# Performance work log

Measured on AMD Instinct MI355X. Metric: run time of the kernel, lower is better.

## Reference

```python
import jax, jax.numpy as jnp
import numpy as np

N_PAPER = 100000
N_AUTHOR = 50000
D = 128
UNITS = 128
E = 500000


def setup_inputs() -> dict:
    key = jax.random.key(0)
    ks = jax.random.split(key, 10)
    s = 1.0 / np.sqrt(D)
    return {
        "x_paper": jax.random.normal(ks[0], (N_PAPER, D), jnp.float32),
        "x_author": jax.random.normal(ks[1], (N_AUTHOR, D), jnp.float32),
        "W_cites": jax.random.normal(ks[2], (D, UNITS), jnp.float32) * s,
        "W_writes": jax.random.normal(ks[3], (D, UNITS), jnp.float32) * s,
        "W_self": jax.random.normal(ks[4], (D, UNITS), jnp.float32) * s,
        "bias": jnp.zeros((UNITS,), jnp.float32),
        "cites_src": jax.random.randint(ks[5], (E,), 0, N_PAPER, jnp.int32),
        "cites_dst": jax.random.randint(ks[6], (E,), 0, N_PAPER, jnp.int32),
        "writes_src": jax.random.randint(ks[7], (E,), 0, N_AUTHOR, jnp.int32),
        "writes_dst": jax.random.randint(ks[8], (E,), 0, N_PAPER, jnp.int32),
    }


def reference(x_paper, x_author, W_cites, W_writes, W_self, bias,
              cites_src, cites_dst, writes_src, writes_dst) -> jnp.ndarray:
    n_recv = x_paper.shape[0]

    # Per-edge-set: transform sender node states, gather to edges, segment-sum to receivers.
    def pool(x_sender, W, src, dst):
        h = x_sender @ W                                  # [n_sender, units]
        msgs = jnp.take(h, src, axis=0)                   # [E, units] broadcast to edges
        pooled = jax.ops.segment_sum(msgs, dst, num_segments=n_recv)
        deg = jax.ops.segment_sum(jnp.ones_like(dst, jnp.float32), dst,
                                  num_segments=n_recv)
        return pooled, deg

    pooled_c, deg_c = pool(x_paper, W_cites, cites_src, cites_dst)
    pooled_w, deg_w = pool(x_author, W_writes, writes_src, writes_dst)

    # Self-loop transform counts as one more "in-edge" per node for mean.
    self_vals = x_paper @ W_self                          # [n_recv, units]
    summed = pooled_c + pooled_w + self_vals
    total_deg = deg_c + deg_w + 1.0                       # [n_recv]

    # tf.math.divide_no_nan semantics
    mean = jnp.where(total_deg[:, None] != 0.0, summed / total_deg[:, None], 0.0)
    return jax.nn.relu(mean + bias)
```

## Files before the change

kernel.cpp:

```cpp
#include <hip/hip_runtime.h>
#include <hip/hip_bf16.h>

#define NP     100000
#define NA     50000
#define DIM    128
#define UNITS  128
#define NEDGE  500000
#define NE2    (2 * NEDGE)

#define BM   128
#define GPB  ((NP + BM - 1) / BM)
#define GAB  ((NA + BM - 1) / BM)

#define CHUNK  1024
#define NCHUNK ((NP + CHUNK - 1) / CHUNK)

typedef __attribute__((ext_vector_type(8))) short bfrag;
typedef __attribute__((ext_vector_type(4))) float f32x4;

__device__ __forceinline__ unsigned int bf_rne(float x) {
    unsigned int u = __builtin_bit_cast(unsigned int, x);
    u += 0x7FFFu + ((u >> 16) & 1u);
    return u >> 16;
}
__device__ __forceinline__ float bf_to_f(unsigned int b) {
    unsigned int u = b << 16;
    return __builtin_bit_cast(float, u);
}

__global__ __launch_bounds__(256, 1) void mfma_gemm_all(
    const float* __restrict__ x_paper, const float* __restrict__ x_author,
    const float* __restrict__ W_cites, const float* __restrict__ W_writes,
    const float* __restrict__ W_self,
    float* __restrict__ H, float* __restrict__ out)
{
    const float* X; const float* W; float* Ho; int nrows; int bb;
    if (blockIdx.x < GPB) {
        X = x_paper;  W = W_cites;  Ho = H;                      nrows = NP; bb = blockIdx.x;
    } else if (blockIdx.x < GPB + GAB) {
        X = x_author; W = W_writes; Ho = H + (size_t)NP * UNITS; nrows = NA; bb = blockIdx.x - GPB;
    } else {
        X = x_paper;  W = W_self;   Ho = out;                    nrows = NP; bb = blockIdx.x - GPB - GAB;
    }

    __shared__ unsigned short Xhi[BM * DIM];
    __shared__ unsigned short Xlo[BM * DIM];
    __shared__ unsigned short Whi[DIM * UNITS];
    __shared__ unsigned short Wlo[DIM * UNITS];

    const int tid  = threadIdx.x;
    const int row0 = bb * BM;

#pragma unroll
    for (int i = 0; i < 8; ++i) {
        const int item = i * 256 + tid;
        const int n    = item & 127;
        const int koct = item >> 7;
        unsigned int h[8], l[8];
#pragma unroll
        for (int j = 0; j < 8; ++j) {
            const float e = W[(size_t)(koct * 8 + j) * UNITS + n];
            h[j] = bf_rne(e);
            l[j] = bf_rne(e - bf_to_f(h[j]));
        }
        uint4 hv, lv;
        hv.x = h[0] | (h[1] << 16); hv.y = h[2] | (h[3] << 16);
        hv.z = h[4] | (h[5] << 16); hv.w = h[6] | (h[7] << 16);
        lv.x = l[0] | (l[1] << 16); lv.y = l[2] | (l[3] << 16);
        lv.z = l[4] | (l[5] << 16); lv.w = l[6] | (l[7] << 16);
        const int slot = koct * 128 + n;
        ((uint4*)Whi)[slot] = hv;
        ((uint4*)Wlo)[slot] = lv;
    }

    const float4* X4 = (const float4*)(X + (size_t)row0 * DIM);
#pragma unroll
    for (int i = 0; i < 8; ++i) {
        const int item = i * 256 + tid;
        const int koct = item & 15;
        const int row  = item >> 4;
        if (row0 + row < nrows) {
            const float4 v0 = X4[row * 32 + koct * 2];
            const float4 v1 = X4[row * 32 + koct * 2 + 1];
            const float e[8] = {v0.x, v0.y, v0.z, v0.w, v1.x, v1.y, v1.z, v1.w};
            unsigned int h[8], l[8];
#pragma unroll
            for (int j = 0; j < 8; ++j) {
                h[j] = bf_rne(e[j]);
                l[j] = bf_rne(e[j] - bf_to_f(h[j]));
            }
            uint4 hv, lv;
            hv.x = h[0] | (h[1] << 16); hv.y = h[2] | (h[3] << 16);
            hv.z = h[4] | (h[5] << 16); hv.w = h[6] | (h[7] << 16);
            lv.x = l[0] | (l[1] << 16); lv.y = l[2] | (l[3] << 16);
            lv.z = l[4] | (l[5] << 16); lv.w = l[6] | (l[7] << 16);
            const int slot = koct * 128 + (row ^ koct);
            ((uint4*)Xhi)[slot] = hv;
            ((uint4*)Xlo)[slot] = lv;
        }
    }
    __syncthreads();

    const int lane = tid & 63;
    const int wv   = tid >> 6;
    const int wr   = (wv >> 1) * 64;
    const int wc   = (wv & 1) * 64;
    const int l16  = lane & 15;
    const int q    = lane >> 4;

    f32x4 acc[4][4];
#pragma unroll
    for (int rt = 0; rt < 4; ++rt)
#pragma unroll
        for (int ct = 0; ct < 4; ++ct) acc[rt][ct] = (f32x4)(0.0f);

#pragma unroll
    for (int kk = 0; kk < 4; ++kk) {
        const int fb = kk * 4 + q;
        bfrag ah[4], al[4], bh[4], bl[4];
#pragma unroll
        for (int rt = 0; rt < 4; ++rt) {
            const int row = wr + rt * 16 + l16;
            const int off = (fb * 128 + (row ^ fb)) * 8;
            ah[rt] = *(const bfrag*)&Xhi[off];
            al[rt] = *(const bfrag*)&Xlo[off];
        }
#pragma unroll
        for (int ct = 0; ct < 4; ++ct) {
            const int off = (fb * 128 + wc + ct * 16 + l16) * 8;
            bh[ct] = *(const bfrag*)&Whi[off];
            bl[ct] = *(const bfrag*)&Wlo[off];
        }
#pragma unroll
        for (int rt = 0; rt < 4; ++rt)
#pragma unroll
            for (int ct = 0; ct < 4; ++ct) {
                acc[rt][ct] = __builtin_amdgcn_mfma_f32_16x16x32_bf16(
                    ah[rt], bh[ct], acc[rt][ct], 0, 0, 0);
                acc[rt][ct] = __builtin_amdgcn_mfma_f32_16x16x32_bf16(
                    ah[rt], bl[ct], acc[rt][ct], 0, 0, 0);
                acc[rt][ct] = __builtin_amdgcn_mfma_f32_16x16x32_bf16(
                    al[rt], bh[ct], acc[rt][ct], 0, 0, 0);
            }
    }

#pragma unroll
    for (int rt = 0; rt < 4; ++rt) {
#pragma unroll
        for (int r = 0; r < 4; ++r) {
            const int row = wr + rt * 16 + q * 4 + r;
            if (row0 + row < nrows) {
                float* dst = Ho + (size_t)(row0 + row) * UNITS + wc + l16;
#pragma unroll
                for (int ct = 0; ct < 4; ++ct) dst[ct * 16] = acc[rt][ct][r];
            }
        }
    }
}

__global__ __launch_bounds__(256) void zero_count(int* __restrict__ count)
{
    int i = blockIdx.x * 256 + threadIdx.x;
    if (i < NP) count[i] = 0;
}

__global__ __launch_bounds__(256) void hist_k(
    const int* __restrict__ c_dst, const int* __restrict__ w_dst,
    int* __restrict__ count)
{
    int i = blockIdx.x * 256 + threadIdx.x;
    if (i >= NE2) return;
    int d = (i < NEDGE) ? c_dst[i] : w_dst[i - NEDGE];
    atomicAdd(&count[d], 1);
}

__global__ __launch_bounds__(256) void scanA(
    const int* __restrict__ count, int* __restrict__ csum)
{
    __shared__ int red[256];
    const int c = blockIdx.x, t = threadIdx.x;
    const int base = c * CHUNK + t * 4;
    int s = 0;
#pragma unroll
    for (int r = 0; r < 4; ++r)
        if (base + r < NP) s += count[base + r];
    red[t] = s; __syncthreads();
#pragma unroll
    for (int off = 128; off > 0; off >>= 1) {
        if (t < off) red[t] += red[t + off];
        __syncthreads();
    }
    if (t == 0) csum[c] = red[0];
}

__global__ __launch_bounds__(128) void scanB(
    const int* __restrict__ csum, int* __restrict__ coff)
{
    __shared__ int ts[128];
    const int t = threadIdx.x;
    const int v = (t < NCHUNK) ? csum[t] : 0;
    ts[t] = v; __syncthreads();
    for (int off = 1; off < 128; off <<= 1) {
        int x = (t >= off) ? ts[t - off] : 0;
        __syncthreads();
        ts[t] += x;
        __syncthreads();
    }
    if (t < NCHUNK) coff[t] = ts[t] - v;
}

__global__ __launch_bounds__(256) void scanC(
    const int* __restrict__ count, const int* __restrict__ coff,
    int* __restrict__ cursor)
{
    __shared__ int ts[256];
    const int c = blockIdx.x, t = threadIdx.x;
    const int base = c * CHUNK + t * 4;
    int v0 = 0, v1 = 0, v2 = 0, v3 = 0;
    if (base + 0 < NP) v0 = count[base + 0];
    if (base + 1 < NP) v1 = count[base + 1];
    if (base + 2 < NP) v2 = count[base + 2];
    if (base + 3 < NP) v3 = count[base + 3];
    const int s = v0 + v1 + v2 + v3;
    ts[t] = s; __syncthreads();
    for (int off = 1; off < 256; off <<= 1) {
        int x = (t >= off) ? ts[t - off] : 0;
        __syncthreads();
        ts[t] += x;
        __syncthreads();
    }
    int excl = ts[t] - s + coff[c];
    if (base + 0 < NP) cursor[base + 0] = excl;
    if (base + 1 < NP) cursor[base + 1] = excl + v0;
    if (base + 2 < NP) cursor[base + 2] = excl + v0 + v1;
    if (base + 3 < NP) cursor[base + 3] = excl + v0 + v1 + v2;
}

__global__ __launch_bounds__(256) void fill_k(
    const int* __restrict__ c_src, const int* __restrict__ c_dst,
    const int* __restrict__ w_src, const int* __restrict__ w_dst,
    int* __restrict__ cursor, int* __restrict__ eidx)
{
    int i = blockIdx.x * 256 + threadIdx.x;
    if (i >= NE2) return;
    int d, val;
    if (i < NEDGE) { d = c_dst[i];         val = c_src[i]; }
    else           { int j = i - NEDGE; d = w_dst[j]; val = NP + w_src[j]; }
    int pos = atomicAdd(&cursor[d], 1);
    eidx[pos] = val;
}

__global__ __launch_bounds__(256) void gather_fused(
    const float* __restrict__ H, const int* __restrict__ eidx,
    const int* __restrict__ cursor, const float* __restrict__ bias,
    float* __restrict__ out)
{
    const int tid = threadIdx.x;
    const int g = tid >> 5, l = tid & 31;
    const int n = blockIdx.x * 8 + g;

    float4 acc = ((const float4*)out)[(size_t)n * 32 + l];

    const int start = (n == 0) ? 0 : cursor[n - 1];
    const int end   = cursor[n];
    const float4* H4 = (const float4*)H;
    int e_next = (start < end) ? eidx[start] : 0;
    for (int j = start; j < end; ++j) {
        const int e = e_next;
        if (j + 1 < end) e_next = eidx[j + 1];
        const float4 v = H4[(size_t)e * 32 + l];
        acc.x += v.x; acc.y += v.y; acc.z += v.z; acc.w += v.w;
    }

    const float inv = 1.0f / (float)(end - start + 1);
    const float4 b = ((const float4*)bias)[l];
    float4 o;
    o.x = fmaxf(fmaf(acc.x, inv, b.x), 0.0f);
    o.y = fmaxf(fmaf(acc.y, inv, b.y), 0.0f);
    o.z = fmaxf(fmaf(acc.z, inv, b.z), 0.0f);
    o.w = fmaxf(fmaf(acc.w, inv, b.w), 0.0f);
    ((float4*)out)[(size_t)n * 32 + l] = o;
}

extern "C" void kernel_launch(void* const* d_in, const int* in_sizes, int n_in,
                              void* d_out, int out_size, void* d_ws, size_t ws_size,
                              hipStream_t stream)
{
    const float* x_paper    = (const float*)d_in[0];
    const float* x_author   = (const float*)d_in[1];
    const float* W_cites    = (const float*)d_in[2];
    const float* W_writes   = (const float*)d_in[3];
    const float* W_self     = (const float*)d_in[4];
    const float* bias       = (const float*)d_in[5];
    const int*   cites_src  = (const int*)d_in[6];
    const int*   cites_dst  = (const int*)d_in[7];
    const int*   writes_src = (const int*)d_in[8];
    const int*   writes_dst = (const int*)d_in[9];
    float* out = (float*)d_out;

    char* ws = (char*)d_ws;
    float* H      = (float*)(ws);
    int*   eidx   = (int*)(ws + 76800000);
    int*   count  = (int*)(ws + 80800000);
    int*   cursor = (int*)(ws + 81200000);
    int*   csum   = (int*)(ws + 81600000);
    int*   coff   = (int*)(ws + 81600512);

    mfma_gemm_all<<<2 * GPB + GAB, 256, 0, stream>>>(
        x_paper, x_author, W_cites, W_writes, W_self, H, out);

    zero_count<<<(NP + 255) / 256, 256, 0, stream>>>(count);
    hist_k<<<(NE2 + 255) / 256, 256, 0, stream>>>(cites_dst, writes_dst, count);
    scanA<<<NCHUNK, 256, 0, stream>>>(count, csum);
    scanB<<<1, 128, 0, stream>>>(csum, coff);
    scanC<<<NCHUNK, 256, 0, stream>>>(count, coff, cursor);
    fill_k<<<(NE2 + 255) / 256, 256, 0, stream>>>(
        cites_src, cites_dst, writes_src, writes_dst, cursor, eidx);

    gather_fused<<<NP / 8, 256, 0, stream>>>(H, eidx, cursor, bias, out);
}
```

Measured before the change: 393.9 us.

## Prepack weights once, load via global_load_lds, merge scan kernels, unroll gather

A new small kernel converts each weight matrix into split-bf16 hi/lo form once and also zeroes the histogram counts. The GEMM blocks then copy the packed weights straight into LDS with global_load_lds instead of each block redoing the float-to-bf16 split. The middle scan pass is folded into the final scan kernel, where every block recomputes the chunk-offset prefix, removing a launch. The gather loop is unrolled by two with two accumulators to keep more loads in flight. The cost is an extra workspace buffer and redundant per-block prefix work.

```diff
diff --git a/kernel.cpp b/kernel.cpp
--- a/kernel.cpp
+++ b/kernel.cpp
@@ -18,6 +18,9 @@
 typedef __attribute__((ext_vector_type(8))) short bfrag;
 typedef __attribute__((ext_vector_type(4))) float f32x4;
 
+typedef const __attribute__((address_space(1))) unsigned int* gptr_u32;
+typedef __attribute__((address_space(3))) unsigned int*       lptr_u32;
+
 __device__ __forceinline__ unsigned int bf_rne(float x) {
     unsigned int u = __builtin_bit_cast(unsigned int, x);
     u += 0x7FFFu + ((u >> 16) & 1u);
@@ -27,50 +30,77 @@
     unsigned int u = b << 16;
     return __builtin_bit_cast(float, u);
 }
+__device__ __forceinline__ void gload_lds16(const void* g, void* l) {
+    __builtin_amdgcn_global_load_lds((gptr_u32)g, (lptr_u32)l, 16, 0, 0);
+}
+
+__global__ __launch_bounds__(256) void wpack_zero(
+    const float* __restrict__ W_cites, const float* __restrict__ W_writes,
+    const float* __restrict__ W_self,
+    unsigned short* __restrict__ Wpk, int* __restrict__ count)
+{
+    const int b = blockIdx.x;
+    if (b < 3) {
+        const float* W = (b == 0) ? W_cites : (b == 1) ? W_writes : W_self;
+        uint4* dst = (uint4*)(Wpk + (size_t)b * 32768);
+        const int tid = threadIdx.x;
+#pragma unroll
+        for (int i = 0; i < 8; ++i) {
+            const int item = i * 256 + tid;
+            const int n    = item & 127;
+            const int koct = item >> 7;
+            unsigned int h[8], l[8];
+#pragma unroll
+            for (int j = 0; j < 8; ++j) {
+                const float e = W[(size_t)(koct * 8 + j) * UNITS + n];
+                h[j] = bf_rne(e);
+                l[j] = bf_rne(e - bf_to_f(h[j]));
+            }
+            uint4 hv, lv;
+            hv.x = h[0] | (h[1] << 16); hv.y = h[2] | (h[3] << 16);
+            hv.z = h[4] | (h[5] << 16); hv.w = h[6] | (h[7] << 16);
+            lv.x = l[0] | (l[1] << 16); lv.y = l[2] | (l[3] << 16);
+            lv.z = l[4] | (l[5] << 16); lv.w = l[6] | (l[7] << 16);
+            dst[koct * 128 + n]        = hv;
+            dst[2048 + koct * 128 + n] = lv;
+        }
+    } else {
+        const int i = (b - 3) * 256 + threadIdx.x;
+        if (i < NP) count[i] = 0;
+    }
+}
 
 __global__ __launch_bounds__(256, 1) void mfma_gemm_all(
     const float* __restrict__ x_paper, const float* __restrict__ x_author,
-    const float* __restrict__ W_cites, const float* __restrict__ W_writes,
-    const float* __restrict__ W_self,
+    const unsigned short* __restrict__ Wpk,
     float* __restrict__ H, float* __restrict__ out)
 {
-    const float* X; const float* W; float* Ho; int nrows; int bb;
+    const float* X; float* Ho; int nrows; int bb; int wid;
     if (blockIdx.x < GPB) {
-        X = x_paper;  W = W_cites;  Ho = H;                      nrows = NP; bb = blockIdx.x;
+        X = x_paper;  Ho = H;                      nrows = NP; bb = blockIdx.x;             wid = 0;
     } else if (blockIdx.x < GPB + GAB) {
-        X = x_author; W = W_writes; Ho = H + (size_t)NP * UNITS; nrows = NA; bb = blockIdx.x - GPB;
+        X = x_author; Ho = H + (size_t)NP * UNITS; nrows = NA; bb = blockIdx.x - GPB;       wid = 1;
     } else {
-        X = x_paper;  W = W_self;   Ho = out;                    nrows = NP; bb = blockIdx.x - GPB - GAB;
+        X = x_paper;  Ho = out;                    nrows = NP; bb = blockIdx.x - GPB - GAB; wid = 2;
     }
 
     __shared__ unsigned short Xhi[BM * DIM];
     __shared__ unsigned short Xlo[BM * DIM];
-    __shared__ unsigned short Whi[DIM * UNITS];
-    __shared__ unsigned short Wlo[DIM * UNITS];
+    __shared__ unsigned short Wl[2 * DIM * UNITS];
 
     const int tid  = threadIdx.x;
+    const int lane = tid & 63;
+    const int wv   = tid >> 6;
     const int row0 = bb * BM;
 
-#pragma unroll
-    for (int i = 0; i < 8; ++i) {
-        const int item = i * 256 + tid;
-        const int n    = item & 127;
-        const int koct = item >> 7;
-        unsigned int h[8], l[8];
-#pragma unroll
-        for (int j = 0; j < 8; ++j) {
-            const float e = W[(size_t)(koct * 8 + j) * UNITS + n];
-            h[j] = bf_rne(e);
-            l[j] = bf_rne(e - bf_to_f(h[j]));
-        }
-        uint4 hv, lv;
-        hv.x = h[0] | (h[1] << 16); hv.y = h[2] | (h[3] << 16);
-        hv.z = h[4] | (h[5] << 16); hv.w = h[6] | (h[7] << 16);
-        lv.x = l[0] | (l[1] << 16); lv.y = l[2] | (l[3] << 16);
-        lv.z = l[4] | (l[5] << 16); lv.w = l[6] | (l[7] << 16);
-        const int slot = koct * 128 + n;
-        ((uint4*)Whi)[slot] = hv;
-        ((uint4*)Wlo)[slot] = lv;
+    {
+        const char* gW = (const char*)Wpk + (size_t)wid * 65536;
+        char*       lW = (char*)Wl;
+#pragma unroll
+        for (int i = 0; i < 16; ++i) {
+            const int off = wv * 16384 + i * 1024;
+            gload_lds16(gW + off + lane * 16, lW + off);
+        }
     }
 
     const float4* X4 = (const float4*)(X + (size_t)row0 * DIM);
@@ -101,12 +131,10 @@
     }
     __syncthreads();
 
-    const int lane = tid & 63;
-    const int wv   = tid >> 6;
-    const int wr   = (wv >> 1) * 64;
-    const int wc   = (wv & 1) * 64;
-    const int l16  = lane & 15;
-    const int q    = lane >> 4;
+    const int wr  = (wv >> 1) * 64;
+    const int wc  = (wv & 1) * 64;
+    const int l16 = lane & 15;
+    const int q   = lane >> 4;
 
     f32x4 acc[4][4];
 #pragma unroll
@@ -128,8 +156,8 @@
 #pragma unroll
         for (int ct = 0; ct < 4; ++ct) {
             const int off = (fb * 128 + wc + ct * 16 + l16) * 8;
-            bh[ct] = *(const bfrag*)&Whi[off];
-            bl[ct] = *(const bfrag*)&Wlo[off];
+            bh[ct] = *(const bfrag*)&Wl[off];
+            bl[ct] = *(const bfrag*)&Wl[16384 + off];
         }
 #pragma unroll
         for (int rt = 0; rt < 4; ++rt)
@@ -158,12 +186,6 @@
     }
 }
 
-__global__ __launch_bounds__(256) void zero_count(int* __restrict__ count)
-{
-    int i = blockIdx.x * 256 + threadIdx.x;
-    if (i < NP) count[i] = 0;
-}
-
 __global__ __launch_bounds__(256) void hist_k(
     const int* __restrict__ c_dst, const int* __restrict__ w_dst,
     int* __restrict__ count)
@@ -193,28 +215,25 @@
     if (t == 0) csum[c] = red[0];
 }
 
-__global__ __launch_bounds__(128) void scanB(
-    const int* __restrict__ csum, int* __restrict__ coff)
-{
-    __shared__ int ts[128];
-    const int t = threadIdx.x;
-    const int v = (t < NCHUNK) ? csum[t] : 0;
-    ts[t] = v; __syncthreads();
-    for (int off = 1; off < 128; off <<= 1) {
-        int x = (t >= off) ? ts[t - off] : 0;
-        __syncthreads();
-        ts[t] += x;
-        __syncthreads();
-    }
-    if (t < NCHUNK) coff[t] = ts[t] - v;
-}
-
-__global__ __launch_bounds__(256) void scanC(
-    const int* __restrict__ count, const int* __restrict__ coff,
+__global__ __launch_bounds__(256) void scanC2(
+    const int* __restrict__ count, const int* __restrict__ csum,
     int* __restrict__ cursor)
 {
+    __shared__ int bs[128];
     __shared__ int ts[256];
     const int c = blockIdx.x, t = threadIdx.x;
+
+    if (t < 128) bs[t] = (t < NCHUNK) ? csum[t] : 0;
+    __syncthreads();
+    for (int off = 1; off < 128; off <<= 1) {
+        int x = 0;
+        if (t < 128 && t >= off) x = bs[t - off];
+        __syncthreads();
+        if (t < 128) bs[t] += x;
+        __syncthreads();
+    }
+    const int coffc = (c == 0) ? 0 : bs[c - 1];
+
     const int base = c * CHUNK + t * 4;
     int v0 = 0, v1 = 0, v2 = 0, v3 = 0;
     if (base + 0 < NP) v0 = count[base + 0];
@@ -229,7 +248,7 @@
         ts[t] += x;
         __syncthreads();
     }
-    int excl = ts[t] - s + coff[c];
+    int excl = ts[t] - s + coffc;
     if (base + 0 < NP) cursor[base + 0] = excl;
     if (base + 1 < NP) cursor[base + 1] = excl + v0;
     if (base + 2 < NP) cursor[base + 2] = excl + v0 + v1;
@@ -260,17 +279,26 @@
     const int n = blockIdx.x * 8 + g;
 
     float4 acc = ((const float4*)out)[(size_t)n * 32 + l];
+    float4 acc2; acc2.x = acc2.y = acc2.z = acc2.w = 0.0f;
 
     const int start = (n == 0) ? 0 : cursor[n - 1];
     const int end   = cursor[n];
     const float4* H4 = (const float4*)H;
-    int e_next = (start < end) ? eidx[start] : 0;
-    for (int j = start; j < end; ++j) {
-        const int e = e_next;
-        if (j + 1 < end) e_next = eidx[j + 1];
-        const float4 v = H4[(size_t)e * 32 + l];
+
+    int j = start;
+    for (; j + 2 <= end; j += 2) {
+        const int e0 = eidx[j];
+        const int e1 = eidx[j + 1];
+        const float4 v0 = H4[(size_t)e0 * 32 + l];
+        const float4 v1 = H4[(size_t)e1 * 32 + l];
+        acc.x  += v0.x; acc.y  += v0.y; acc.z  += v0.z; acc.w  += v0.w;
+        acc2.x += v1.x; acc2.y += v1.y; acc2.z += v1.z; acc2.w += v1.w;
+    }
+    if (j < end) {
+        const float4 v = H4[(size_t)eidx[j] * 32 + l];
         acc.x += v.x; acc.y += v.y; acc.z += v.z; acc.w += v.w;
     }
+    acc.x += acc2.x; acc.y += acc2.y; acc.z += acc2.z; acc.w += acc2.w;
 
     const float inv = 1.0f / (float)(end - start + 1);
     const float4 b = ((const float4*)bias)[l];
@@ -299,21 +327,22 @@
     float* out = (float*)d_out;
 
     char* ws = (char*)d_ws;
-    float* H      = (float*)(ws);
-    int*   eidx   = (int*)(ws + 76800000);
-    int*   count  = (int*)(ws + 80800000);
-    int*   cursor = (int*)(ws + 81200000);
-    int*   csum   = (int*)(ws + 81600000);
-    int*   coff   = (int*)(ws + 81600512);
+    float*          H      = (float*)(ws);
+    int*            eidx   = (int*)(ws + 76800000);
+    int*            count  = (int*)(ws + 80800000);
+    int*            cursor = (int*)(ws + 81200000);
+    int*            csum   = (int*)(ws + 81600000);
+    unsigned short* Wpk    = (unsigned short*)(ws + 81601024);
+
+    wpack_zero<<<3 + (NP + 255) / 256, 256, 0, stream>>>(
+        W_cites, W_writes, W_self, Wpk, count);
 
     mfma_gemm_all<<<2 * GPB + GAB, 256, 0, stream>>>(
-        x_paper, x_author, W_cites, W_writes, W_self, H, out);
-
-    zero_count<<<(NP + 255) / 256, 256, 0, stream>>>(count);
+        x_paper, x_author, Wpk, H, out);
+
     hist_k<<<(NE2 + 255) / 256, 256, 0, stream>>>(cites_dst, writes_dst, count);
     scanA<<<NCHUNK, 256, 0, stream>>>(count, csum);
-    scanB<<<1, 128, 0, stream>>>(csum, coff);
-    scanC<<<NCHUNK, 256, 0, stream>>>(count, coff, cursor);
+    scanC2<<<NCHUNK, 256, 0, stream>>>(count, csum, cursor);
     fill_k<<<(NE2 + 255) / 256, 256, 0, stream>>>(
         cites_src, cites_dst, writes_src, writes_dst, cursor, eidx);
 
```

Measured after the change: 387.5 us. Within noise of the previous version (-1.6%).
